# Kernel optimization log

Hardware: AMD Instinct MI355X
Metric: run time of the kernel (lower is better)

## Reference

```python
import jax, jax.numpy as jnp
import numpy as np

NCLUSTER = 512
NC = 3

def setup_inputs() -> dict:
    key = jax.random.key(0)
    k1, k2 = jax.random.split(key)
    x = jax.random.normal(k1, (4, NC, 256, 256), dtype=jnp.float32)
    C = jax.random.normal(k2, (NCLUSTER, NC), dtype=jnp.float32)
    return {"x": x, "C": C}

def reference(x, C):
    # x: [bs, c, h, w]; C: [ncluster, c]
    bs, c, h, w = x.shape
    xf = x.reshape(bs, c, h * w).transpose(0, 2, 1)  # [bs, HW, c]
    d = ((xf ** 2).sum(-1, keepdims=True)
         - 2.0 * jnp.einsum('bnc,kc->bnk', xf, C)
         + (C ** 2).sum(-1))
    a = jnp.argmin(d, axis=-1)  # [bs, HW] codebook indices
    return a
```

## Files before the change

### kernel.cpp

```cpp
#include <hip/hip_runtime.h>

#define NCLUSTER 512
#define NC 3
#define HW 65536
#define BLOCK 256
#define NW 4
#define KSUB (NCLUSTER / NW)
#define PPT 2
#define PXB (64 * PPT)
#define EPS 1e-4f

__global__ __launch_bounds__(BLOCK) void kmeans_assign(
    const float* __restrict__ x,
    const float* __restrict__ C,
    int* __restrict__ out)
{
    __shared__ float4 lc[NCLUSTER];
    __shared__ float  rb1[NW][PXB];
    __shared__ float  rb2[NW][PXB];
    __shared__ int    ridx[NW][PXB];
    __shared__ int    qpx[PXB];
    __shared__ int    qcnt;

    if (threadIdx.x == 0) qcnt = 0;
    for (int k = threadIdx.x; k < NCLUSTER; k += BLOCK) {
        double c0 = C[k * NC + 0];
        double c1 = C[k * NC + 1];
        double c2 = C[k * NC + 2];
        lc[k] = make_float4((float)c0, (float)c1, (float)c2,
                            (float)(0.5 * (c0 * c0 + c1 * c1 + c2 * c2)));
    }
    __syncthreads();

    const int w = threadIdx.x >> 6;
    const int l = threadIdx.x & 63;
    const int B0 = blockIdx.x * PXB;
    const int pB = B0 & (HW - 1);
    const float* xb = x + (size_t)(B0 >> 16) * NC * HW;

    float x0[PPT], x1[PPT], x2[PPT], b1[PPT], b2[PPT];
    int id[PPT];
#pragma unroll
    for (int i = 0; i < PPT; ++i) {
        int p = pB + l + i * 64;
        x0[i] = xb[p];
        x1[i] = xb[p + HW];
        x2[i] = xb[p + 2 * HW];
        b1[i] = 1e30f;
        b2[i] = 1e30f;
        id[i] = 0;
    }

    const int k0 = w * KSUB;
#pragma unroll 4
    for (int k = 0; k < KSUB; ++k) {
        float4 c = lc[k0 + k];
#pragma unroll
        for (int i = 0; i < PPT; ++i) {
            float t = __builtin_fmaf(-x0[i], c.x, c.w);
            t = __builtin_fmaf(-x1[i], c.y, t);
            t = __builtin_fmaf(-x2[i], c.z, t);
            bool lt = t < b1[i];
            b2[i] = __builtin_amdgcn_fmed3f(t, b1[i], b2[i]);
            id[i] = lt ? (k0 + k) : id[i];
            b1[i] = fminf(t, b1[i]);
        }
    }

#pragma unroll
    for (int i = 0; i < PPT; ++i) {
        rb1[w][l + i * 64] = b1[i];
        rb2[w][l + i * 64] = b2[i];
        ridx[w][l + i * 64] = id[i];
    }
    __syncthreads();

    if (threadIdx.x < PXB) {
        const int t = threadIdx.x;
        float g1m = rb1[0][t];
        float g2m = rb2[0][t];
        int gi = ridx[0][t];
#pragma unroll
        for (int ww = 1; ww < NW; ++ww) {
            float a1 = rb1[ww][t];
            float a2 = rb2[ww][t];
            int ai = ridx[ww][t];
            bool lt = a1 < g1m;
            g2m = lt ? fminf(g1m, a2) : fminf(g2m, a1);
            gi = lt ? ai : gi;
            g1m = fminf(g1m, a1);
        }
        if (g2m - g1m < EPS) {
            qpx[atomicAdd(&qcnt, 1)] = t;
        } else {
            out[B0 + t] = gi;
        }
    }
    __syncthreads();

    const int n = qcnt;
    for (int e = w; e < n; e += NW) {
        const int t = qpx[e];
        const int p = pB + t;
        double X0 = (double)xb[p];
        double X1 = (double)xb[p + HW];
        double X2 = (double)xb[p + 2 * HW];
        double bd = 1e300;
        int bi = 0;
#pragma unroll
        for (int j = 0; j < NCLUSTER / 64; ++j) {
            int k = j * 64 + l;
            float4 c = lc[k];
            double d0 = X0 - (double)c.x;
            double d1 = X1 - (double)c.y;
            double d2 = X2 - (double)c.z;
            double d = d0 * d0 + d1 * d1 + d2 * d2;
            if (d < bd) { bd = d; bi = k; }
        }
#pragma unroll
        for (int m = 1; m < 64; m <<= 1) {
            double od = __shfl_xor(bd, m, 64);
            int oi = __shfl_xor(bi, m, 64);
            bool take = (od < bd) || (od == bd && oi < bi);
            bd = take ? od : bd;
            bi = take ? oi : bi;
        }
        if (l == 0) out[B0 + t] = bi;
    }
}

extern "C" void kernel_launch(void* const* d_in, const int* in_sizes, int n_in,
                              void* d_out, int out_size, void* d_ws, size_t ws_size,
                              hipStream_t stream) {
    const float* x = (const float*)d_in[0];
    const float* C = (const float*)d_in[1];
    int* out = (int*)d_out;

    int total = out_size;
    int grid = total / PXB;
    kmeans_assign<<<grid, BLOCK, 0, stream>>>(x, C, out);
}
```

Measured before the change: 33.48 us.

## Use packed FP32 FMA over pixel pairs and enlarge per-thread pixel tile

Each thread now handles eight pixels instead of two, and the block grows to 512 threads (eight waves, each scanning 64 clusters). Pixels are handled in pairs, and the three distance FMAs per pair are issued as v_pk_fma_f32 through inline asm. For this, the centroid table is split into two float2 LDS arrays, and pixel coordinates are pre-negated. The aim is to halve FMA issue and spread each LDS centroid read over more pixels. In exchange, register pressure rises and the grid has far fewer blocks, which may leave CUs underfilled or reduce occupancy.

```diff
diff --git a/kernel.cpp b/kernel.cpp
--- a/kernel.cpp
+++ b/kernel.cpp
@@ -3,67 +3,88 @@
 #define NCLUSTER 512
 #define NC 3
 #define HW 65536
-#define BLOCK 256
-#define NW 4
+#define BLOCK 512
+#define NW 8
 #define KSUB (NCLUSTER / NW)
-#define PPT 2
-#define PXB (64 * PPT)
+#define PPT 8
+#define NPAIR (PPT / 2)
 #define EPS 1e-4f
 
-__global__ __launch_bounds__(BLOCK) void kmeans_assign(
+typedef float f32x2 __attribute__((ext_vector_type(2)));
+
+__global__ __launch_bounds__(BLOCK, 4) void kmeans_assign(
     const float* __restrict__ x,
     const float* __restrict__ C,
     int* __restrict__ out)
 {
-    __shared__ float4 lc[NCLUSTER];
-    __shared__ float  rb1[NW][PXB];
-    __shared__ float  rb2[NW][PXB];
-    __shared__ int    ridx[NW][PXB];
-    __shared__ int    qpx[PXB];
-    __shared__ int    qcnt;
+    __shared__ f32x2 lcA[NCLUSTER];
+    __shared__ f32x2 lcB[NCLUSTER];
+    __shared__ float rb1[NW][BLOCK];
+    __shared__ float rb2[NW][BLOCK];
+    __shared__ int   ridx[NW][BLOCK];
+    __shared__ int   qpx[BLOCK];
+    __shared__ int   qcnt;
 
     if (threadIdx.x == 0) qcnt = 0;
     for (int k = threadIdx.x; k < NCLUSTER; k += BLOCK) {
         double c0 = C[k * NC + 0];
         double c1 = C[k * NC + 1];
         double c2 = C[k * NC + 2];
-        lc[k] = make_float4((float)c0, (float)c1, (float)c2,
-                            (float)(0.5 * (c0 * c0 + c1 * c1 + c2 * c2)));
+        lcA[k] = (f32x2){(float)c0, (float)c1};
+        lcB[k] = (f32x2){(float)c2, (float)(0.5 * (c0 * c0 + c1 * c1 + c2 * c2))};
     }
     __syncthreads();
 
     const int w = threadIdx.x >> 6;
     const int l = threadIdx.x & 63;
-    const int B0 = blockIdx.x * PXB;
+    const int B0 = blockIdx.x * BLOCK;
     const int pB = B0 & (HW - 1);
     const float* xb = x + (size_t)(B0 >> 16) * NC * HW;
 
-    float x0[PPT], x1[PPT], x2[PPT], b1[PPT], b2[PPT];
+    f32x2 NX0[NPAIR], NX1[NPAIR], NX2[NPAIR];
+    float b1[PPT], b2[PPT];
     int id[PPT];
 #pragma unroll
-    for (int i = 0; i < PPT; ++i) {
-        int p = pB + l + i * 64;
-        x0[i] = xb[p];
-        x1[i] = xb[p + HW];
-        x2[i] = xb[p + 2 * HW];
-        b1[i] = 1e30f;
-        b2[i] = 1e30f;
-        id[i] = 0;
+    for (int j = 0; j < NPAIR; ++j) {
+        int pa = pB + l + j * 128;
+        int pc = pa + 64;
+        NX0[j] = (f32x2){-xb[pa], -xb[pc]};
+        NX1[j] = (f32x2){-xb[pa + HW], -xb[pc + HW]};
+        NX2[j] = (f32x2){-xb[pa + 2 * HW], -xb[pc + 2 * HW]};
     }
+#pragma unroll
+    for (int i = 0; i < PPT; ++i) { b1[i] = 1e30f; b2[i] = 1e30f; id[i] = 0; }
 
     const int k0 = w * KSUB;
-#pragma unroll 4
+#pragma unroll 2
     for (int k = 0; k < KSUB; ++k) {
-        float4 c = lc[k0 + k];
+        f32x2 cA = lcA[k0 + k];
+        f32x2 cB = lcB[k0 + k];
+        const int kk = k0 + k;
 #pragma unroll
-        for (int i = 0; i < PPT; ++i) {
-            float t = __builtin_fmaf(-x0[i], c.x, c.w);
-            t = __builtin_fmaf(-x1[i], c.y, t);
-            t = __builtin_fmaf(-x2[i], c.z, t);
-            bool lt = t < b1[i];
-            b2[i] = __builtin_amdgcn_fmed3f(t, b1[i], b2[i]);
-            id[i] = lt ? (k0 + k) : id[i];
-            b1[i] = fminf(t, b1[i]);
+        for (int j = 0; j < NPAIR; ++j) {
+            f32x2 T;
+            asm("v_pk_fma_f32 %0, %1, %2, %3 op_sel:[0,0,1] op_sel_hi:[1,0,1]"
+                : "=v"(T) : "v"(NX0[j]), "v"(cA), "v"(cB));
+            asm("v_pk_fma_f32 %0, %1, %2, %0 op_sel:[0,1,0] op_sel_hi:[1,1,1]"
+                : "+v"(T) : "v"(NX1[j]), "v"(cA));
+            asm("v_pk_fma_f32 %0, %1, %2, %0 op_sel:[0,0,0] op_sel_hi:[1,0,1]"
+                : "+v"(T) : "v"(NX2[j]), "v"(cB));
+            float t0 = T.x, t1 = T.y;
+            {
+                const int i = 2 * j;
+                bool lt = t0 < b1[i];
+                b2[i] = __builtin_amdgcn_fmed3f(t0, b1[i], b2[i]);
+                id[i] = lt ? kk : id[i];
+                b1[i] = fminf(t0, b1[i]);
+            }
+            {
+                const int i = 2 * j + 1;
+                bool lt = t1 < b1[i];
+                b2[i] = __builtin_amdgcn_fmed3f(t1, b1[i], b2[i]);
+                id[i] = lt ? kk : id[i];
+                b1[i] = fminf(t1, b1[i]);
+            }
         }
     }
 
@@ -75,7 +96,7 @@
     }
     __syncthreads();
 
-    if (threadIdx.x < PXB) {
+    {
         const int t = threadIdx.x;
         float g1m = rb1[0][t];
         float g2m = rb2[0][t];
@@ -110,10 +131,11 @@
 #pragma unroll
         for (int j = 0; j < NCLUSTER / 64; ++j) {
             int k = j * 64 + l;
-            float4 c = lc[k];
-            double d0 = X0 - (double)c.x;
-            double d1 = X1 - (double)c.y;
-            double d2 = X2 - (double)c.z;
+            f32x2 a = lcA[k];
+            f32x2 b = lcB[k];
+            double d0 = X0 - (double)a.x;
+            double d1 = X1 - (double)a.y;
+            double d2 = X2 - (double)b.x;
             double d = d0 * d0 + d1 * d1 + d2 * d2;
             if (d < bd) { bd = d; bi = k; }
         }
@@ -137,6 +159,6 @@
     int* out = (int*)d_out;
 
     int total = out_size;
-    int grid = total / PXB;
+    int grid = total / BLOCK;
     kmeans_assign<<<grid, BLOCK, 0, stream>>>(x, C, out);
 }
```

Result: slower. 36.86 us (+10.1%).
